# Performance work log

Measured on AMD Instinct MI355X. Metric: run time of the kernel, lower is better.

The kernel has to match this reference:

```python
import jax, jax.numpy as jnp
from jax import lax
import numpy as np

DN = ('NCDHW', 'OIDHW', 'NCDHW')
ACTIVE_THRESH = 1


def setup_inputs() -> dict:
    key = jax.random.key(0)
    ks = jax.random.split(key, 10)
    B, D = 4, 64
    chans = [3, 64, 128, 256, 512]
    inp = {
        'x': jax.random.normal(ks[0], (B, 3, D, D, D), jnp.float32),
        'mask': jax.random.randint(ks[1], (B, D, D, D), 0, 20, jnp.int32),
    }
    for i in range(4):
        cin, cout = chans[i], chans[i + 1]
        fan_in = cin * 27
        scale = 1.0 / np.sqrt(fan_in)
        inp[f'w{i+1}'] = jax.random.normal(ks[2 + 2 * i], (cout, cin, 3, 3, 3), jnp.float32) * scale
        inp[f'b{i+1}'] = jax.random.normal(ks[3 + 2 * i], (cout,), jnp.float32) * scale
    return inp


def _sparse_block(x, m, w, b, stride):
    # SparseConv3d(k=3, pad=1) + SparseReLU: output active where 3^3 footprint hits an active input;
    # bias + relu applied only at active sites, inactive sites stay exactly 0 (spconv .dense() semantics).
    s = (stride,) * 3
    pad = [(1, 1)] * 3
    y = lax.conv_general_dilated(x, w, s, pad, dimension_numbers=DN)
    ones = jnp.ones((1, 1, 3, 3, 3), x.dtype)
    m_out = lax.conv_general_dilated(m[:, None].astype(x.dtype), ones, s, pad, dimension_numbers=DN) > 0
    y = jnp.where(m_out, jax.nn.relu(y + b[None, :, None, None, None]), jnp.zeros((), x.dtype))
    return y, m_out[:, 0]


def reference(x, mask, w1, b1, w2, b2, w3, b3, w4, b4):
    m = mask < ACTIVE_THRESH                       # [B,D,H,W] active voxels
    h = x * m[:, None].astype(x.dtype)             # zero inactive input features
    h, m = _sparse_block(h, m, w1, b1, 1)          # [B,64,64,64,64]
    h, m = _sparse_block(h, m, w2, b2, 2)          # [B,128,32,32,32]
    h, m = _sparse_block(h, m, w3, b3, 2)          # [B,256,16,16,16]
    h, m = _sparse_block(h, m, w4, b4, 2)          # [B,512,8,8,8]
    pooled = jnp.max(h, axis=(2, 3, 4))            # dense() + amax over D,H,W -> [B,512]
    return jax.nn.leaky_relu(pooled, negative_slope=0.2)
```

## Files before the change

kernel.cpp:

```cpp
#include <hip/hip_runtime.h>

typedef _Float16 f16;
typedef _Float16 half4 __attribute__((ext_vector_type(4)));
typedef _Float16 half8 __attribute__((ext_vector_type(8)));
typedef float f32x4 __attribute__((ext_vector_type(4)));

#define BATCH 4

__device__ __forceinline__ void gload16(const void* g, void* l) {
  __builtin_amdgcn_global_load_lds((const __attribute__((address_space(1))) unsigned int*)g,
                                   (__attribute__((address_space(3))) unsigned int*)l, 16, 0, 0);
}

template<int DP, int ROWB>
__global__ __launch_bounds__(256) void zborder_k(char* __restrict__ buf) {
  int v = blockIdx.x * 256 + threadIdx.x;
  int b = blockIdx.y;
  if (v >= DP * DP * DP) return;
  int w = v % DP; int t = v / DP; int h = t % DP; int d = t / DP;
  bool border = (w == 0) | (w == DP - 1) | (h == 0) | (h == DP - 1) | (d == 0) | (d == DP - 1);
  if (!border) return;
  char* p = buf + ((size_t)b * DP * DP * DP + v) * ROWB;
  #pragma unroll
  for (int i = 0; i < ROWB; i += 8)
    *reinterpret_cast<unsigned long long*>(p + i) = 0ull;
}

__global__ __launch_bounds__(256) void wprep_k(const float* __restrict__ w,
                                               f16* __restrict__ w27, int COUT, int CIN) {
  int idx = blockIdx.x * 256 + threadIdx.x;
  int total = COUT * CIN * 27;
  if (idx >= total) return;
  int k = idx % 27;
  int t = idx / 27;
  int ci = t % CIN;
  int co = t / CIN;
  w27[((size_t)k * COUT + co) * CIN + ci] = (f16)w[idx];
}

__global__ __launch_bounds__(256) void wprep1_k(const float* __restrict__ w,
                                                f16* __restrict__ wf) {
  int idx = blockIdx.x * 256 + threadIdx.x;
  if (idx >= 64 * 128) return;
  int q = idx & 127, co = idx >> 7;
  int k = q >> 2, ci = q & 3;
  float v = (ci < 3 && k < 27) ? w[(co * 3 + ci) * 27 + k] : 0.f;
  wf[idx] = (f16)v;
}

__global__ __launch_bounds__(256) void xmask_k(const float* __restrict__ x,
                                               const int* __restrict__ mask,
                                               f16* __restrict__ xcp) {
  const int D3 = 262144, PD = 66, PD3 = PD * PD * PD;
  int pv = blockIdx.x * 256 + threadIdx.x;
  if (pv >= PD3) return;
  int b = blockIdx.y;
  int pw = pv % PD; int t = pv / PD; int ph = t % PD; int pd = t / PD;
  half4 o = {};
  if (pw > 0 && pw < 65 && ph > 0 && ph < 65 && pd > 0 && pd < 65) {
    int v = (((pd - 1) * 64) + (ph - 1)) * 64 + (pw - 1);
    bool act = mask[(size_t)b * D3 + v] < 1;
    if (act) {
      const float* xb = x + (size_t)b * 3 * D3 + v;
      o[0] = (f16)xb[0];
      o[1] = (f16)xb[D3];
      o[2] = (f16)xb[2 * D3];
    }
  }
  *reinterpret_cast<half4*>(xcp + ((size_t)b * PD3 + pv) * 4) = o;
}

__global__ __launch_bounds__(256) void dil_w_k(const int* __restrict__ mask,
                                               unsigned char* __restrict__ aw) {
  const int D3 = 262144;
  int t = blockIdx.x * 256 + threadIdx.x;
  int b = t >> 16;
  int v = (t & 65535) * 4;
  int w0 = v & 63;
  const int* mb = mask + (size_t)b * D3;
  int a[6];
  a[0] = (w0 > 0) ? (mb[v - 1] < 1) : 0;
  #pragma unroll
  for (int i = 0; i < 4; i++) a[i + 1] = mb[v + i] < 1;
  a[5] = (w0 < 60) ? (mb[v + 4] < 1) : 0;
  unsigned int o = 0;
  #pragma unroll
  for (int i = 0; i < 4; i++)
    o |= ((unsigned)(a[i] | a[i + 1] | a[i + 2])) << (8 * i);
  *reinterpret_cast<unsigned int*>(aw + (size_t)b * D3 + v) = o;
}

template<int STRIDE, int DIMSHIFT>
__global__ __launch_bounds__(256) void dil_hd_k(const unsigned char* __restrict__ ai,
                                                unsigned char* __restrict__ ao) {
  const int D3 = 262144;
  int t = blockIdx.x * 256 + threadIdx.x;
  int b = t >> 16;
  int v = (t & 65535) * 4;
  int c = (v >> DIMSHIFT) & 63;
  const unsigned char* ib = ai + (size_t)b * D3;
  unsigned int m = *reinterpret_cast<const unsigned int*>(ib + v);
  if (c > 0)  m |= *reinterpret_cast<const unsigned int*>(ib + v - STRIDE);
  if (c < 63) m |= *reinterpret_cast<const unsigned int*>(ib + v + STRIDE);
  *reinterpret_cast<unsigned int*>(ao + (size_t)b * D3 + v) = m;
}

template<int DIN, int DOUT>
__global__ __launch_bounds__(256) void dilate_s2_k(const unsigned char* __restrict__ mi,
                                                   unsigned char* __restrict__ mo) {
  const int Do3 = DOUT * DOUT * DOUT;
  int v = blockIdx.x * 256 + threadIdx.x;
  if (v >= Do3) return;
  int b = blockIdx.y;
  int ow = v % DOUT, t = v / DOUT, oh = t % DOUT, od = t / DOUT;
  const unsigned char* ib = mi + (size_t)b * DIN * DIN * DIN;
  int act = 0;
  for (int kd = 0; kd < 3; kd++) { int id = od * 2 - 1 + kd; if ((unsigned)id >= (unsigned)DIN) continue;
    for (int kh = 0; kh < 3; kh++) { int ih = oh * 2 - 1 + kh; if ((unsigned)ih >= (unsigned)DIN) continue;
      for (int kw = 0; kw < 3; kw++) { int iw = ow * 2 - 1 + kw; if ((unsigned)iw >= (unsigned)DIN) continue;
        act |= ib[((size_t)id * DIN + ih) * DIN + iw];
      } } }
  mo[(size_t)b * Do3 + v] = (unsigned char)(act ? 1 : 0);
}

template<int BM>
__global__ __launch_bounds__(256) void conv1_mfma_k(const f16* __restrict__ xcp,
                                                    const f16* __restrict__ w1f,
                                                    const float* __restrict__ bias,
                                                    const unsigned char* __restrict__ mo,
                                                    f16* __restrict__ out ) {
  const int D3 = 262144, COUT = 64, PD = 66, PD3 = PD * PD * PD;
  constexpr int K = 128, LD = K + 8;
  constexpr int WM = 2, WN = 2;
  constexpr int MF = BM / (16 * WM), NF = 64 / (16 * WN);
  __shared__ __align__(16) f16 As[BM][LD];
  __shared__ __align__(16) f16 Bs[64][LD];

  const int tid = threadIdx.x, lane = tid & 63, wave = tid >> 6;
  const int wm = wave >> 1, wn = wave & 1;
  const int v0 = blockIdx.x * BM;
  const int b = blockIdx.y;
  const f16* xb = xcp + (size_t)b * PD3 * 4;

  for (int c = tid; c < 64 * (K / 8); c += 256) {
    int row = c >> 4, cc = c & 15;
    *reinterpret_cast<half8*>(&Bs[row][cc * 8]) =
        *reinterpret_cast<const half8*>(w1f + row * K + cc * 8);
  }
  {
    const int row = tid & (BM - 1);
    const int v = v0 + row;
    const int ow = v & 63, oh = (v >> 6) & 63, od = v >> 12;
    const int base = (od * PD + oh) * PD + ow;
    for (int e = tid; e < 32 * BM; e += 256) {
      int kslot = e / BM;
      half4 val = {};
      if (kslot < 27) {
        int kd = kslot / 9, r2 = kslot - kd * 9, kh = r2 / 3, kw = r2 - kh * 3;
        val = *reinterpret_cast<const half4*>(xb + (size_t)(base + (kd * PD + kh) * PD + kw) * 4);
      }
      *reinterpret_cast<half4*>(&As[row][kslot * 4]) = val;
    }
  }
  __syncthreads();

  f32x4 acc[MF][NF] = {};
  const int chanoff = (lane >> 4) << 3;
  const int arow = wm * MF * 16 + (lane & 15);
  const int brow = wn * NF * 16 + (lane & 15);
  #pragma unroll
  for (int q0 = 0; q0 < K; q0 += 32) {
    half8 a[MF], bb[NF];
    #pragma unroll
    for (int mf = 0; mf < MF; mf++)
      a[mf] = *reinterpret_cast<const half8*>(&As[arow + mf * 16][q0 + chanoff]);
    #pragma unroll
    for (int nf = 0; nf < NF; nf++)
      bb[nf] = *reinterpret_cast<const half8*>(&Bs[brow + nf * 16][q0 + chanoff]);
    #pragma unroll
    for (int mf = 0; mf < MF; mf++)
      #pragma unroll
      for (int nf = 0; nf < NF; nf++)
        acc[mf][nf] = __builtin_amdgcn_mfma_f32_16x16x32_f16(a[mf], bb[nf], acc[mf][nf], 0, 0, 0);
  }

  const unsigned char* mb = mo + (size_t)b * D3;
  f16* ob = out + (size_t)b * PD3 * COUT;
  const int ll = lane & 15, lh = lane >> 4;
  float bv[NF];
  #pragma unroll
  for (int nf = 0; nf < NF; nf++) bv[nf] = bias[wn * NF * 16 + nf * 16 + ll];
  #pragma unroll
  for (int mf = 0; mf < MF; mf++) {
    #pragma unroll
    for (int r = 0; r < 4; r++) {
      int v = v0 + wm * MF * 16 + mf * 16 + (lh << 2) + r;
      bool act = mb[v] != 0;
      int ow = v & 63, oh = (v >> 6) & 63, od = v >> 12;
      size_t pv = ((size_t)(od + 1) * PD + oh + 1) * PD + ow + 1;
      #pragma unroll
      for (int nf = 0; nf < NF; nf++) {
        int co = wn * NF * 16 + nf * 16 + ll;
        float val = acc[mf][nf][r] + bv[nf];
        val = act ? (val > 0.f ? val : 0.f) : 0.f;
        ob[pv * COUT + co] = (f16)val;
      }
    }
  }
}

template<int CINS, int CINF, int COUT, int DIN, int DOUT, int BM, int BN,
         int WM, int WN, int SWZ, int OP, int BMERGE>
__global__ __launch_bounds__(WM * WN * 64) void conv_mfma2_k(const f16* __restrict__ in,
                                                             const f16* __restrict__ w27,
                                                             const float* __restrict__ bias,
                                                             const unsigned char* __restrict__ mo,
                                                             f16* __restrict__ out) {
  constexpr int PD = DIN + 2, PDo = DOUT + 2;
  constexpr int NW = WM * WN;
  constexpr int MF = BM / (16 * WM), NF = BN / (16 * WN);
  constexpr int ROWB = CINS * 2;
  constexpr int ROWBF = CINF * 2;
  constexpr int CHUNKS = ROWB / 16;
  constexpr int RPI = 64 / CHUNKS;
  constexpr int A_IW = BM / RPI / NW;
  constexpr int B_IW = BN / RPI / NW;
  constexpr int CIH = CINF / CINS;
  constexpr int NSTEP = 27 * CIH;
  constexpr int CI0S = CINS / 32;
  constexpr int D3o = DOUT * DOUT * DOUT;
  constexpr int LOGD = (DOUT == 32) ? 5 : ((DOUT == 16) ? 4 : 3);

  __shared__ __align__(16) char As[2][BM * ROWB];
  __shared__ __align__(16) char Bs[2][BN * ROWB];

  const int tid = threadIdx.x, lane = tid & 63, wave = tid >> 6;
  const int wm = wave / WN, wn = wave % WN;
  int bx = blockIdx.x;
  if (SWZ) {
    int cpx = gridDim.x >> 3;
    bx = (bx & 7) * cpx + (bx >> 3);
  }
  const int v0 = bx * BM, co0 = blockIdx.y * BN;
  const int bz = BMERGE ? 0 : blockIdx.z;

  auto key = [](int r) -> int { return (CHUNKS >= 8) ? (r & 7) : ((r >> 1) & 3); };

  const int lrow = lane / CHUNKS;
  const int lchunk = lane % CHUNKS;
  const char* a_src[A_IW];
  #pragma unroll
  for (int i = 0; i < A_IW; i++) {
    int r = (wave * A_IW + i) * RPI + lrow;
    int v = v0 + r;
    int vb = BMERGE ? (v >> (3 * LOGD)) : bz;
    int vv = BMERGE ? (v & (D3o - 1)) : v;
    int ow = vv & (DOUT - 1), oh = (vv >> LOGD) & (DOUT - 1), od = vv >> (2 * LOGD);
    size_t flat = (size_t)vb * PD * PD * PD + ((size_t)(2 * od) * PD + 2 * oh) * PD + 2 * ow;
    a_src[i] = (const char*)in + flat * ROWBF + (lchunk ^ key(r)) * 16;
  }
  const char* b_src[B_IW];
  #pragma unroll
  for (int i = 0; i < B_IW; i++) {
    int r = (wave * B_IW + i) * RPI + lrow;
    b_src[i] = (const char*)w27 + (size_t)(co0 + r) * ROWBF + (lchunk ^ key(r)) * 16;
  }

  auto stage = [&](int buf, int s) {
    int k = s / CIH;
    int h = s - k * CIH;
    int kd = k / 9, r2 = k - kd * 9, kh = r2 / 3, kw = r2 - kh * 3;
    int koff = ((kd * PD + kh) * PD + kw) * ROWBF + h * ROWB;
    #pragma unroll
    for (int i = 0; i < A_IW; i++)
      gload16(a_src[i] + koff, &As[buf][(wave * A_IW + i) * 1024]);
    size_t wko = (size_t)k * COUT * ROWBF + h * ROWB;
    #pragma unroll
    for (int i = 0; i < B_IW; i++)
      gload16(b_src[i] + wko, &Bs[buf][(wave * B_IW + i) * 1024]);
  };

  f32x4 acc[MF][NF] = {};
  const int ll = lane & 15, lh = lane >> 4;
  const int ra0 = wm * MF * 16 + ll;
  const int rb0 = wn * NF * 16 + ll;
  const int rswa = key(ra0);
  const int rswb = key(rb0);

  stage(0, 0);
  __syncthreads();
  int cur = 0;
  for (int s = 0; s < NSTEP; s++) {
    if (s < NSTEP - 1) stage(cur ^ 1, s + 1);
    #pragma unroll
    for (int c = 0; c < CI0S; c++) {
      const int q = c * 4 + lh;
      half8 a[MF], bb[NF];
      #pragma unroll
      for (int mf = 0; mf < MF; mf++)
        a[mf] = *reinterpret_cast<const half8*>(
            &As[cur][(ra0 + mf * 16) * ROWB + ((q ^ rswa) * 16)]);
      #pragma unroll
      for (int nf = 0; nf < NF; nf++)
        bb[nf] = *reinterpret_cast<const half8*>(
            &Bs[cur][(rb0 + nf * 16) * ROWB + ((q ^ rswb) * 16)]);
      #pragma unroll
      for (int mf = 0; mf < MF; mf++)
        #pragma unroll
        for (int nf = 0; nf < NF; nf++)
          acc[mf][nf] = __builtin_amdgcn_mfma_f32_16x16x32_f16(a[mf], bb[nf], acc[mf][nf], 0, 0, 0);
    }
    __syncthreads();
    cur ^= 1;
  }

  f16* ob = out;
  float bv[NF];
  #pragma unroll
  for (int nf = 0; nf < NF; nf++) bv[nf] = bias[co0 + wn * NF * 16 + nf * 16 + ll];
  #pragma unroll
  for (int mf = 0; mf < MF; mf++) {
    #pragma unroll
    for (int r = 0; r < 4; r++) {
      int v = v0 + wm * MF * 16 + mf * 16 + (lh << 2) + r;
      int vb = BMERGE ? (v >> (3 * LOGD)) : bz;
      int vv = BMERGE ? (v & (D3o - 1)) : v;
      bool act = mo[(size_t)vb * D3o + vv] != 0;
      int ow = vv & (DOUT - 1), oh = (vv >> LOGD) & (DOUT - 1), od = vv >> (2 * LOGD);
      size_t pv = OP ? (((size_t)(od + 1) * PDo + oh + 1) * PDo + ow + 1) : (size_t)vv;
      size_t obase = ((size_t)vb * (OP ? PDo * PDo * PDo : D3o) + pv) * COUT;
      #pragma unroll
      for (int nf = 0; nf < NF; nf++) {
        int co = co0 + wn * NF * 16 + nf * 16 + ll;
        float val = acc[mf][nf][r] + bv[nf];
        val = act ? (val > 0.f ? val : 0.f) : 0.f;
        ob[obase + co] = (f16)val;
      }
    }
  }
}

__global__ __launch_bounds__(256) void pool_k(const f16* __restrict__ h4,
                                              float* __restrict__ outp) {
  __shared__ float red[4][64];
  int b = blockIdx.y;
  int cl = threadIdx.x & 63;
  int co = blockIdx.x * 64 + cl;
  int vg = threadIdx.x >> 6;
  const f16* p = h4 + (size_t)b * 512 * 512;
  float m = 0.f;
  for (int v = vg * 128; v < vg * 128 + 128; v++) m = fmaxf(m, (float)p[(size_t)v * 512 + co]);
  red[vg][cl] = m;
  __syncthreads();
  if (threadIdx.x < 64) {
    m = fmaxf(fmaxf(red[0][threadIdx.x], red[1][threadIdx.x]),
              fmaxf(red[2][threadIdx.x], red[3][threadIdx.x]));
    float r = (m >= 0.f) ? m : 0.2f * m;
    outp[b * 512 + blockIdx.x * 64 + threadIdx.x] = r;
  }
}

extern "C" void kernel_launch(void* const* d_in, const int* in_sizes, int n_in,
                              void* d_out, int out_size, void* d_ws, size_t ws_size,
                              hipStream_t stream) {
  const float* x    = (const float*)d_in[0];
  const int*   mask = (const int*)d_in[1];
  const float* w1 = (const float*)d_in[2];
  const float* b1 = (const float*)d_in[3];
  const float* w2 = (const float*)d_in[4];
  const float* b2 = (const float*)d_in[5];
  const float* w3 = (const float*)d_in[6];
  const float* b3 = (const float*)d_in[7];
  const float* w4 = (const float*)d_in[8];
  const float* b4 = (const float*)d_in[9];
  float* outp = (float*)d_out;

  const size_t PD1 = 66 * 66 * 66;
  const size_t PD2 = 34 * 34 * 34;
  const size_t PD3s = 18 * 18 * 18;

  char* ws = (char*)d_ws;
  size_t off = 0;
  auto alloc = [&](size_t bytes) -> char* {
    char* p = ws + off;
    off = (off + bytes + 255) & ~(size_t)255;
    return p;
  };
  f16* wf1 = (f16*)alloc((size_t)64 * 128 * 2);
  f16* wf2 = (f16*)alloc((size_t)27 * 128 * 64 * 2);
  f16* wf3 = (f16*)alloc((size_t)27 * 256 * 128 * 2);
  f16* wf4 = (f16*)alloc((size_t)27 * 512 * 256 * 2);
  unsigned char* aw = (unsigned char*)alloc((size_t)BATCH * 262144);
  unsigned char* ah = (unsigned char*)alloc((size_t)BATCH * 262144);
  unsigned char* m1 = (unsigned char*)alloc((size_t)BATCH * 262144);
  unsigned char* m2 = (unsigned char*)alloc((size_t)BATCH * 32768);
  unsigned char* m3 = (unsigned char*)alloc((size_t)BATCH * 4096);
  unsigned char* m4 = (unsigned char*)alloc((size_t)BATCH * 512);
  f16* h1p = (f16*)alloc((size_t)BATCH * PD1 * 64 * 2);
  f16* h2p = (f16*)alloc((size_t)BATCH * PD2 * 128 * 2);
  f16* h3p = (f16*)alloc((size_t)BATCH * PD3s * 256 * 2);
  f16* h4  = (f16*)alloc((size_t)BATCH * 512 * 512 * 2);
  f16* xcp = h3p;
  if (off > ws_size) return;

  wprep1_k<<<dim3((64 * 128 + 255) / 256), 256, 0, stream>>>(w1, wf1);
  wprep_k<<<dim3((128 * 64 * 27 + 255) / 256), 256, 0, stream>>>(w2, wf2, 128, 64);
  wprep_k<<<dim3((256 * 128 * 27 + 255) / 256), 256, 0, stream>>>(w3, wf3, 256, 128);
  wprep_k<<<dim3((512 * 256 * 27 + 255) / 256), 256, 0, stream>>>(w4, wf4, 512, 256);

  dil_w_k<<<dim3(BATCH * 65536 / 256), 256, 0, stream>>>(mask, aw);
  dil_hd_k<64, 6><<<dim3(BATCH * 65536 / 256), 256, 0, stream>>>(aw, ah);
  dil_hd_k<4096, 12><<<dim3(BATCH * 65536 / 256), 256, 0, stream>>>(ah, m1);
  dilate_s2_k<64, 32><<<dim3(128, BATCH), 256, 0, stream>>>(m1, m2);
  dilate_s2_k<32, 16><<<dim3(16, BATCH), 256, 0, stream>>>(m2, m3);
  dilate_s2_k<16, 8><<<dim3(2, BATCH), 256, 0, stream>>>(m3, m4);

  xmask_k<<<dim3((287496 + 255) / 256, BATCH), 256, 0, stream>>>(x, mask, xcp);
  zborder_k<66, 128><<<dim3((287496 + 255) / 256, BATCH), 256, 0, stream>>>((char*)h1p);
  zborder_k<34, 256><<<dim3((39304 + 255) / 256, BATCH), 256, 0, stream>>>((char*)h2p);

  conv1_mfma_k<128><<<dim3(262144 / 128, BATCH), 256, 0, stream>>>(xcp, wf1, b1, m1, h1p);

  zborder_k<18, 512><<<dim3((5832 + 255) / 256, BATCH), 256, 0, stream>>>((char*)h3p);

  conv_mfma2_k<64, 64, 128, 64, 32, 64, 128, 2, 2, 1, 1, 0>
      <<<dim3(512, 1, BATCH), 256, 0, stream>>>(h1p, wf2, b2, m2, h2p);
  conv_mfma2_k<64, 128, 256, 32, 16, 64, 128, 2, 2, 1, 1, 1>
      <<<dim3(256, 2, 1), 256, 0, stream>>>(h2p, wf3, b3, m3, h3p);
  conv_mfma2_k<128, 256, 512, 16, 8, 32, 64, 1, 2, 0, 0, 0>
      <<<dim3(16, 8, BATCH), 128, 0, stream>>>(h3p, wf4, b4, m4, h4);

  pool_k<<<dim3(8, BATCH), 256, 0, stream>>>(h4, outp);
}
```

Before: 352.1 us.

## Add 8-wave 4-buffer pipelined conv kernel for layer 2

Adds a new conv kernel that uses 8 waves (2x4) and a 128x128 tile. It runs a 4-buffer, 3-deep async global-to-LDS prefetch pipeline with explicit vmcnt waits, interleaves the next-stage loads between the MFMA chunks, and raises wave priority around the MFMAs. Layer 2 switches to this kernel with half as many blocks. The aim is to hide global-load latency and improve reuse per block, at the cost of much more LDS per block (128 KB), which may limit occupancy.

```diff
diff --git a/kernel.cpp b/kernel.cpp
--- a/kernel.cpp
+++ b/kernel.cpp
@@ -10,6 +10,15 @@
 __device__ __forceinline__ void gload16(const void* g, void* l) {
   __builtin_amdgcn_global_load_lds((const __attribute__((address_space(1))) unsigned int*)g,
                                    (__attribute__((address_space(3))) unsigned int*)l, 16, 0, 0);
+}
+
+template<int N> __device__ __forceinline__ void wait_vmcnt() {
+  static_assert(N == 0 || N == 4 || N == 8 || N == 12 || N == 16, "add literal");
+  if constexpr (N == 0)       asm volatile("s_waitcnt vmcnt(0)" ::: "memory");
+  else if constexpr (N == 4)  asm volatile("s_waitcnt vmcnt(4)" ::: "memory");
+  else if constexpr (N == 8)  asm volatile("s_waitcnt vmcnt(8)" ::: "memory");
+  else if constexpr (N == 12) asm volatile("s_waitcnt vmcnt(12)" ::: "memory");
+  else if constexpr (N == 16) asm volatile("s_waitcnt vmcnt(16)" ::: "memory");
 }
 
 template<int DP, int ROWB>
@@ -204,6 +213,145 @@
         float val = acc[mf][nf][r] + bv[nf];
         val = act ? (val > 0.f ? val : 0.f) : 0.f;
         ob[pv * COUT + co] = (f16)val;
+      }
+    }
+  }
+}
+
+template<int CIN, int COUT, int DIN, int DOUT, int BM, int BN, int SWZ, int OP>
+__global__ __launch_bounds__(512) void conv_8p_k(const f16* __restrict__ in,
+                                                 const f16* __restrict__ w27,
+                                                 const float* __restrict__ bias,
+                                                 const unsigned char* __restrict__ mo,
+                                                 f16* __restrict__ out) {
+  constexpr int PD = DIN + 2, PDo = DOUT + 2;
+  constexpr int NW = 8, WM = 2, WN = 4;
+  constexpr int MF = BM / (16 * WM), NF = BN / (16 * WN);
+  constexpr int ROWB = CIN * 2;
+  constexpr int CHUNKS = ROWB / 16;
+  constexpr int RPI = 64 / CHUNKS;
+  constexpr int A_IW = BM / RPI / NW;
+  constexpr int B_IW = BN / RPI / NW;
+  constexpr int L = A_IW + B_IW;
+  constexpr int NBUF = 4, DEP = 3;
+  constexpr int CI0S = CIN / 32;
+  constexpr int D3o = DOUT * DOUT * DOUT;
+  constexpr int LOGD = (DOUT == 32) ? 5 : ((DOUT == 16) ? 4 : 3);
+
+  __shared__ __align__(16) char As[NBUF][BM * ROWB];
+  __shared__ __align__(16) char Bs[NBUF][BN * ROWB];
+
+  const int tid = threadIdx.x, lane = tid & 63, wave = tid >> 6;
+  const int wm = wave >> 2, wn = wave & 3;
+  int bx = blockIdx.x;
+  if (SWZ) {
+    int cpx = gridDim.x >> 3;
+    bx = (bx & 7) * cpx + (bx >> 3);
+  }
+  const int v0 = bx * BM, co0 = blockIdx.y * BN, bz = blockIdx.z;
+
+  const int lrow = lane / CHUNKS;
+  const int lchunk = lane % CHUNKS;
+  const char* a_src[A_IW];
+  #pragma unroll
+  for (int i = 0; i < A_IW; i++) {
+    int r = (wave * A_IW + i) * RPI + lrow;
+    int v = v0 + r;
+    int ow = v & (DOUT - 1), oh = (v >> LOGD) & (DOUT - 1), od = v >> (2 * LOGD);
+    size_t flat = (size_t)bz * PD * PD * PD + ((size_t)(2 * od) * PD + 2 * oh) * PD + 2 * ow;
+    a_src[i] = (const char*)in + flat * ROWB + (lchunk ^ (r & 7)) * 16;
+  }
+  const char* b_src[B_IW];
+  #pragma unroll
+  for (int i = 0; i < B_IW; i++) {
+    int r = (wave * B_IW + i) * RPI + lrow;
+    b_src[i] = (const char*)w27 + (size_t)(co0 + r) * ROWB + (lchunk ^ (r & 7)) * 16;
+  }
+
+  auto stageA = [&](int buf, int k) {
+    int kd = k / 9, r2 = k - kd * 9, kh = r2 / 3, kw = r2 - kh * 3;
+    int koff = ((kd * PD + kh) * PD + kw) * ROWB;
+    #pragma unroll
+    for (int i = 0; i < A_IW; i++)
+      gload16(a_src[i] + koff, &As[buf][(wave * A_IW + i) * 1024]);
+  };
+  auto stageB = [&](int buf, int k) {
+    size_t wko = (size_t)k * COUT * ROWB;
+    #pragma unroll
+    for (int i = 0; i < B_IW; i++)
+      gload16(b_src[i] + wko, &Bs[buf][(wave * B_IW + i) * 1024]);
+  };
+
+  f32x4 acc[MF][NF] = {};
+  const int ll = lane & 15, lh = lane >> 4;
+  const int ra0 = wm * MF * 16 + ll;
+  const int rb0 = wn * NF * 16 + ll;
+  const int rswa = ra0 & 7;
+  const int rswb = rb0 & 7;
+
+  stageA(0, 0); stageB(0, 0);
+  stageA(1, 1); stageB(1, 1);
+  stageA(2, 2); stageB(2, 2);
+
+  int cur = 0;
+  for (int s = 0; s < 27; s++) {
+    int rem = 26 - s;
+    if (rem >= 2)      wait_vmcnt<2 * L>();
+    else if (rem == 1) wait_vmcnt<L>();
+    else               wait_vmcnt<0>();
+    __builtin_amdgcn_s_barrier();
+    asm volatile("" ::: "memory");
+    const char* Ab = As[cur];
+    const char* Bb = Bs[cur];
+    int nb = (cur == 0) ? NBUF - 1 : cur - 1;
+    bool pf = (s + DEP) < 27;
+    #pragma unroll
+    for (int c = 0; c < CI0S; c++) {
+      if (c == 0 && pf) stageA(nb, s + DEP);
+      if (c == 1 && pf) stageB(nb, s + DEP);
+      const int q = c * (CHUNKS / CI0S) + lh;
+      half8 a[MF], bb[NF];
+      #pragma unroll
+      for (int mf = 0; mf < MF; mf++)
+        a[mf] = *reinterpret_cast<const half8*>(
+            &Ab[(ra0 + mf * 16) * ROWB + ((q ^ rswa) * 16)]);
+      #pragma unroll
+      for (int nf = 0; nf < NF; nf++)
+        bb[nf] = *reinterpret_cast<const half8*>(
+            &Bb[(rb0 + nf * 16) * ROWB + ((q ^ rswb) * 16)]);
+      __builtin_amdgcn_s_setprio(1);
+      #pragma unroll
+      for (int mf = 0; mf < MF; mf++)
+        #pragma unroll
+        for (int nf = 0; nf < NF; nf++)
+          acc[mf][nf] = __builtin_amdgcn_mfma_f32_16x16x32_f16(a[mf], bb[nf], acc[mf][nf], 0, 0, 0);
+      __builtin_amdgcn_s_setprio(0);
+    }
+    asm volatile("s_waitcnt lgkmcnt(0)" ::: "memory");
+    __builtin_amdgcn_s_barrier();
+    asm volatile("" ::: "memory");
+    cur = (cur + 1 == NBUF) ? 0 : cur + 1;
+  }
+
+  f16* ob = out;
+  float bv[NF];
+  #pragma unroll
+  for (int nf = 0; nf < NF; nf++) bv[nf] = bias[co0 + wn * NF * 16 + nf * 16 + ll];
+  #pragma unroll
+  for (int mf = 0; mf < MF; mf++) {
+    #pragma unroll
+    for (int r = 0; r < 4; r++) {
+      int v = v0 + wm * MF * 16 + mf * 16 + (lh << 2) + r;
+      bool act = mo[(size_t)bz * D3o + v] != 0;
+      int ow = v & (DOUT - 1), oh = (v >> LOGD) & (DOUT - 1), od = v >> (2 * LOGD);
+      size_t pv = OP ? (((size_t)(od + 1) * PDo + oh + 1) * PDo + ow + 1) : (size_t)v;
+      size_t obase = ((size_t)bz * (OP ? PDo * PDo * PDo : D3o) + pv) * COUT;
+      #pragma unroll
+      for (int nf = 0; nf < NF; nf++) {
+        int co = co0 + wn * NF * 16 + nf * 16 + ll;
+        float val = acc[mf][nf][r] + bv[nf];
+        val = act ? (val > 0.f ? val : 0.f) : 0.f;
+        ob[obase + co] = (f16)val;
       }
     }
   }
@@ -423,8 +571,8 @@
 
   zborder_k<18, 512><<<dim3((5832 + 255) / 256, BATCH), 256, 0, stream>>>((char*)h3p);
 
-  conv_mfma2_k<64, 64, 128, 64, 32, 64, 128, 2, 2, 1, 1, 0>
-      <<<dim3(512, 1, BATCH), 256, 0, stream>>>(h1p, wf2, b2, m2, h2p);
+  conv_8p_k<64, 128, 64, 32, 128, 128, 1, 1>
+      <<<dim3(256, 1, BATCH), 512, 0, stream>>>(h1p, wf2, b2, m2, h2p);
   conv_mfma2_k<64, 128, 256, 32, 16, 64, 128, 2, 2, 1, 1, 1>
       <<<dim3(256, 2, 1), 256, 0, stream>>>(h2p, wf3, b3, m3, h3p);
   conv_mfma2_k<128, 256, 512, 16, 8, 32, 64, 1, 2, 0, 0, 0>
```

New measurement: 386.2 us. 9.7% more time.

## Merge prep kernels, compute coarse masks directly, fuse max-pool into conv4

Applied to the files above, without the earlier changes.

Folds the four weight-prep launches into one kernel and replaces the three chained stride-2 mask dilations with one kernel that computes each coarse mask straight from m1 over a widened window. That kernel also zeroes the output. Conv4 now keeps a running max in registers and writes it with atomicMax on the float bits, which removes the h4 buffer and the pool kernel. Launch count and intermediate traffic drop. The atomic trick relies on values being non-negative, since they are post-ReLU and the output starts at 0, but the final leaky_relu step is gone because pooled values are always >= 0. The coarse masks cost more reads per output, with an early exit.

```diff
diff --git a/kernel.cpp b/kernel.cpp
--- a/kernel.cpp
+++ b/kernel.cpp
@@ -26,26 +26,37 @@
     *reinterpret_cast<unsigned long long*>(p + i) = 0ull;
 }
 
-__global__ __launch_bounds__(256) void wprep_k(const float* __restrict__ w,
-                                               f16* __restrict__ w27, int COUT, int CIN) {
+__global__ __launch_bounds__(256) void wprep_all_k(const float* __restrict__ w1,
+                                                   const float* __restrict__ w2,
+                                                   const float* __restrict__ w3,
+                                                   const float* __restrict__ w4,
+                                                   f16* __restrict__ wf1,
+                                                   f16* __restrict__ wf2,
+                                                   f16* __restrict__ wf3,
+                                                   f16* __restrict__ wf4) {
+  const int T1 = 64 * 128;
+  const int T2 = 27 * 128 * 64;
+  const int T3 = 27 * 256 * 128;
+  const int T4 = 27 * 512 * 256;
   int idx = blockIdx.x * 256 + threadIdx.x;
-  int total = COUT * CIN * 27;
-  if (idx >= total) return;
+  if (idx < T1) {
+    int q = idx & 127, co = idx >> 7;
+    int k = q >> 2, ci = q & 3;
+    float v = (ci < 3 && k < 27) ? w1[(co * 3 + ci) * 27 + k] : 0.f;
+    wf1[idx] = (f16)v;
+    return;
+  }
+  idx -= T1;
+  const float* w; f16* wo; int COUT, CIN;
+  if (idx < T2)       { w = w2; wo = wf2; COUT = 128; CIN = 64; }
+  else if ((idx -= T2) < T3) { w = w3; wo = wf3; COUT = 256; CIN = 128; }
+  else if ((idx -= T3) < T4) { w = w4; wo = wf4; COUT = 512; CIN = 256; }
+  else return;
   int k = idx % 27;
   int t = idx / 27;
   int ci = t % CIN;
   int co = t / CIN;
-  w27[((size_t)k * COUT + co) * CIN + ci] = (f16)w[idx];
-}
-
-__global__ __launch_bounds__(256) void wprep1_k(const float* __restrict__ w,
-                                                f16* __restrict__ wf) {
-  int idx = blockIdx.x * 256 + threadIdx.x;
-  if (idx >= 64 * 128) return;
-  int q = idx & 127, co = idx >> 7;
-  int k = q >> 2, ci = q & 3;
-  float v = (ci < 3 && k < 27) ? w[(co * 3 + ci) * 27 + k] : 0.f;
-  wf[idx] = (f16)v;
+  wo[((size_t)k * COUT + co) * CIN + ci] = (f16)w[idx];
 }
 
 __global__ __launch_bounds__(256) void xmask_k(const float* __restrict__ x,
@@ -105,22 +116,36 @@
   *reinterpret_cast<unsigned int*>(ao + (size_t)b * D3 + v) = m;
 }
 
-template<int DIN, int DOUT>
-__global__ __launch_bounds__(256) void dilate_s2_k(const unsigned char* __restrict__ mi,
-                                                   unsigned char* __restrict__ mo) {
-  const int Do3 = DOUT * DOUT * DOUT;
-  int v = blockIdx.x * 256 + threadIdx.x;
-  if (v >= Do3) return;
-  int b = blockIdx.y;
-  int ow = v % DOUT, t = v / DOUT, oh = t % DOUT, od = t / DOUT;
-  const unsigned char* ib = mi + (size_t)b * DIN * DIN * DIN;
+__global__ __launch_bounds__(256) void dil_rest_k(const unsigned char* __restrict__ m1,
+                                                  unsigned char* __restrict__ m2,
+                                                  unsigned char* __restrict__ m3,
+                                                  unsigned char* __restrict__ m4,
+                                                  float* __restrict__ outp) {
+  const int D = 64, D3 = 262144;
+  const int S2 = BATCH * 32768, S3 = BATCH * 4096, S4 = BATCH * 512;
+  int idx = blockIdx.x * 256 + threadIdx.x;
+  int b, v, LOGD, H, ST;
+  unsigned char* mo;
+  if (idx < S2)                 { b = idx >> 15; v = idx & 32767; LOGD = 5; H = 1; ST = 2; mo = m2 + (size_t)b * 32768; }
+  else if ((idx -= S2) < S3)    { b = idx >> 12; v = idx & 4095;  LOGD = 4; H = 3; ST = 4; mo = m3 + (size_t)b * 4096; }
+  else if ((idx -= S3) < S4)    { b = idx >> 9;  v = idx & 511;   LOGD = 3; H = 7; ST = 8; mo = m4 + (size_t)b * 512; }
+  else if ((idx -= S4) < 2048)  { outp[idx] = 0.f; return; }
+  else return;
+  int DM = (1 << LOGD) - 1;
+  int ow = v & DM, oh = (v >> LOGD) & DM, od = v >> (2 * LOGD);
+  const unsigned char* mb = m1 + (size_t)b * D3;
   int act = 0;
-  for (int kd = 0; kd < 3; kd++) { int id = od * 2 - 1 + kd; if ((unsigned)id >= (unsigned)DIN) continue;
-    for (int kh = 0; kh < 3; kh++) { int ih = oh * 2 - 1 + kh; if ((unsigned)ih >= (unsigned)DIN) continue;
-      for (int kw = 0; kw < 3; kw++) { int iw = ow * 2 - 1 + kw; if ((unsigned)iw >= (unsigned)DIN) continue;
-        act |= ib[((size_t)id * DIN + ih) * DIN + iw];
-      } } }
-  mo[(size_t)b * Do3 + v] = (unsigned char)(act ? 1 : 0);
+  for (int dd = -H; dd <= H && !act; dd++) {
+    int id = od * ST + dd; if ((unsigned)id >= (unsigned)D) continue;
+    for (int hh = -H; hh <= H && !act; hh++) {
+      int ih = oh * ST + hh; if ((unsigned)ih >= (unsigned)D) continue;
+      for (int ww = -H; ww <= H; ww++) {
+        int iw = ow * ST + ww; if ((unsigned)iw >= (unsigned)D) continue;
+        if (mb[((size_t)id * D + ih) * D + iw]) { act = 1; break; }
+      }
+    }
+  }
+  mo[v] = (unsigned char)act;
 }
 
 template<int BM>
@@ -210,12 +235,13 @@
 }
 
 template<int CINS, int CINF, int COUT, int DIN, int DOUT, int BM, int BN,
-         int WM, int WN, int SWZ, int OP, int BMERGE>
+         int WM, int WN, int SWZ, int OP, int BMERGE, int POOL>
 __global__ __launch_bounds__(WM * WN * 64) void conv_mfma2_k(const f16* __restrict__ in,
                                                              const f16* __restrict__ w27,
                                                              const float* __restrict__ bias,
                                                              const unsigned char* __restrict__ mo,
-                                                             f16* __restrict__ out) {
+                                                             f16* __restrict__ out,
+                                                             float* __restrict__ poolp) {
   constexpr int PD = DIN + 2, PDo = DOUT + 2;
   constexpr int NW = WM * WN;
   constexpr int MF = BM / (16 * WM), NF = BN / (16 * WN);
@@ -318,6 +344,9 @@
   float bv[NF];
   #pragma unroll
   for (int nf = 0; nf < NF; nf++) bv[nf] = bias[co0 + wn * NF * 16 + nf * 16 + ll];
+  float pmax[NF];
+  #pragma unroll
+  for (int nf = 0; nf < NF; nf++) pmax[nf] = 0.f;
   #pragma unroll
   for (int mf = 0; mf < MF; mf++) {
     #pragma unroll
@@ -334,29 +363,20 @@
         int co = co0 + wn * NF * 16 + nf * 16 + ll;
         float val = acc[mf][nf][r] + bv[nf];
         val = act ? (val > 0.f ? val : 0.f) : 0.f;
-        ob[obase + co] = (f16)val;
+        if constexpr (POOL) {
+          pmax[nf] = fmaxf(pmax[nf], val);
+        } else {
+          ob[obase + co] = (f16)val;
+        }
       }
     }
   }
-}
-
-__global__ __launch_bounds__(256) void pool_k(const f16* __restrict__ h4,
-                                              float* __restrict__ outp) {
-  __shared__ float red[4][64];
-  int b = blockIdx.y;
-  int cl = threadIdx.x & 63;
-  int co = blockIdx.x * 64 + cl;
-  int vg = threadIdx.x >> 6;
-  const f16* p = h4 + (size_t)b * 512 * 512;
-  float m = 0.f;
-  for (int v = vg * 128; v < vg * 128 + 128; v++) m = fmaxf(m, (float)p[(size_t)v * 512 + co]);
-  red[vg][cl] = m;
-  __syncthreads();
-  if (threadIdx.x < 64) {
-    m = fmaxf(fmaxf(red[0][threadIdx.x], red[1][threadIdx.x]),
-              fmaxf(red[2][threadIdx.x], red[3][threadIdx.x]));
-    float r = (m >= 0.f) ? m : 0.2f * m;
-    outp[b * 512 + blockIdx.x * 64 + threadIdx.x] = r;
+  if constexpr (POOL) {
+    #pragma unroll
+    for (int nf = 0; nf < NF; nf++) {
+      int co = co0 + wn * NF * 16 + nf * 16 + ll;
+      atomicMax((int*)poolp + bz * 512 + co, __float_as_int(pmax[nf]));
+    }
   }
 }
 
@@ -399,21 +419,21 @@
   f16* h1p = (f16*)alloc((size_t)BATCH * PD1 * 64 * 2);
   f16* h2p = (f16*)alloc((size_t)BATCH * PD2 * 128 * 2);
   f16* h3p = (f16*)alloc((size_t)BATCH * PD3s * 256 * 2);
-  f16* h4  = (f16*)alloc((size_t)BATCH * 512 * 512 * 2);
   f16* xcp = h3p;
   if (off > ws_size) return;
 
-  wprep1_k<<<dim3((64 * 128 + 255) / 256), 256, 0, stream>>>(w1, wf1);
-  wprep_k<<<dim3((128 * 64 * 27 + 255) / 256), 256, 0, stream>>>(w2, wf2, 128, 64);
-  wprep_k<<<dim3((256 * 128 * 27 + 255) / 256), 256, 0, stream>>>(w3, wf3, 256, 128);
-  wprep_k<<<dim3((512 * 256 * 27 + 255) / 256), 256, 0, stream>>>(w4, wf4, 512, 256);
+  {
+    const int TOT = 64 * 128 + 27 * 128 * 64 + 27 * 256 * 128 + 27 * 512 * 256;
+    wprep_all_k<<<dim3((TOT + 255) / 256), 256, 0, stream>>>(w1, w2, w3, w4, wf1, wf2, wf3, wf4);
+  }
 
   dil_w_k<<<dim3(BATCH * 65536 / 256), 256, 0, stream>>>(mask, aw);
   dil_hd_k<64, 6><<<dim3(BATCH * 65536 / 256), 256, 0, stream>>>(aw, ah);
   dil_hd_k<4096, 12><<<dim3(BATCH * 65536 / 256), 256, 0, stream>>>(ah, m1);
-  dilate_s2_k<64, 32><<<dim3(128, BATCH), 256, 0, stream>>>(m1, m2);
-  dilate_s2_k<32, 16><<<dim3(16, BATCH), 256, 0, stream>>>(m2, m3);
-  dilate_s2_k<16, 8><<<dim3(2, BATCH), 256, 0, stream>>>(m3, m4);
+  {
+    const int TOT = BATCH * 32768 + BATCH * 4096 + BATCH * 512 + 2048;
+    dil_rest_k<<<dim3((TOT + 255) / 256), 256, 0, stream>>>(m1, m2, m3, m4, outp);
+  }
 
   xmask_k<<<dim3((287496 + 255) / 256, BATCH), 256, 0, stream>>>(x, mask, xcp);
   zborder_k<66, 128><<<dim3((287496 + 255) / 256, BATCH), 256, 0, stream>>>((char*)h1p);
@@ -423,12 +443,10 @@
 
   zborder_k<18, 512><<<dim3((5832 + 255) / 256, BATCH), 256, 0, stream>>>((char*)h3p);
 
-  conv_mfma2_k<64, 64, 128, 64, 32, 64, 128, 2, 2, 1, 1, 0>
-      <<<dim3(512, 1, BATCH), 256, 0, stream>>>(h1p, wf2, b2, m2, h2p);
-  conv_mfma2_k<64, 128, 256, 32, 16, 64, 128, 2, 2, 1, 1, 1>
-      <<<dim3(256, 2, 1), 256, 0, stream>>>(h2p, wf3, b3, m3, h3p);
-  conv_mfma2_k<128, 256, 512, 16, 8, 32, 64, 1, 2, 0, 0, 0>
-      <<<dim3(16, 8, BATCH), 128, 0, stream>>>(h3p, wf4, b4, m4, h4);
-
-  pool_k<<<dim3(8, BATCH), 256, 0, stream>>>(h4, outp);
-}
+  conv_mfma2_k<64, 64, 128, 64, 32, 64, 128, 2, 2, 1, 1, 0, 0>
+      <<<dim3(512, 1, BATCH), 256, 0, stream>>>(h1p, wf2, b2, m2, h2p, nullptr);
+  conv_mfma2_k<64, 128, 256, 32, 16, 64, 128, 2, 2, 1, 1, 1, 0>
+      <<<dim3(256, 2, 1), 256, 0, stream>>>(h2p, wf3, b3, m3, h3p, nullptr);
+  conv_mfma2_k<128, 256, 512, 16, 8, 32, 64, 1, 2, 0, 0, 0, 1>
+      <<<dim3(16, 8, BATCH), 128, 0, stream>>>(h3p, wf4, b4, m4, nullptr, outp);
+}
```

Measured after the change: 328.3 us. 1.07x faster.
